# Kernel optimization log

Hardware: AMD Instinct MI355X
Metric: run time of the kernel (lower is better)

Reference implementation:

```python
import jax, jax.numpy as jnp
import numpy as np

BN_EPS = 1e-5

def setup_inputs() -> dict:
    key = jax.random.key(0)
    ks = jax.random.split(key, 6)
    N, D, H = 1024, 256, 128
    scale = 0.05
    return {
        "graph_embeddings": jax.random.normal(ks[0], (N, D), jnp.float32),
        "W1": jax.random.normal(ks[1], (2 * D, H), jnp.float32) * scale,
        "b1": jnp.zeros((H,), jnp.float32),
        "W2": jax.random.normal(ks[2], (H, 1), jnp.float32) * scale,
        "b2": jnp.zeros((1,), jnp.float32),
        "Wg": jax.random.normal(ks[3], (D, H), jnp.float32) * scale,
        "bg": jnp.zeros((H,), jnp.float32),
        "gamma": jnp.ones((H,), jnp.float32),
        "beta": jnp.zeros((H,), jnp.float32),
    }

def reference(graph_embeddings, W1, b1, W2, b2, Wg, bg, gamma, beta):
    N, D = graph_embeddings.shape
    # Pairwise similarity MLP: sim(i,j) = sigmoid(W2 @ relu(W1 @ [x_i; x_j] + b1) + b2)
    # Split W1 over the concat dim so we never materialize [N,N,2D].
    a = graph_embeddings @ W1[:D]          # [N, H] contribution of x_i
    c = graph_embeddings @ W1[D:]          # [N, H] contribution of x_j
    h = jax.nn.relu(a[:, None, :] + c[None, :, :] + b1)   # [N, N, H]
    sim = jax.nn.sigmoid(jnp.einsum('ijh,h->ij', h, W2[:, 0]) + b2[0])  # [N, N]
    # Torch loop uses sim(i,j) with i<j for both directions; keep edge iff sim > 0.5.
    U = jnp.triu(sim, k=1)
    A = jnp.where(U > 0.5, U, 0.0)
    A = A + A.T + jnp.eye(N, dtype=sim.dtype)  # symmetric + GCN self-loops (weight 1)
    # GCN symmetric normalization: D^{-1/2} A D^{-1/2}
    deg = A.sum(axis=1)
    dis = jax.lax.rsqrt(deg)
    A_hat = A * dis[:, None] * dis[None, :]
    out = A_hat @ (graph_embeddings @ Wg) + bg  # [N, H]
    # BatchNorm1d (training mode: batch stats, biased variance)
    mean = out.mean(axis=0)
    var = out.var(axis=0)
    out = gamma * (out - mean) * jax.lax.rsqrt(var + BN_EPS) + beta
    return jax.nn.relu(out)
```

## Files before the change

kernel.cpp:

```cpp
#include <hip/hip_runtime.h>
#include <math.h>

constexpr int NN = 1024;
constexpr int DD = 256;
constexpr int HH = 128;
constexpr float BN_EPS = 1e-5f;

constexpr int OFF_A      = 0;
constexpr int OFF_AP     = OFF_A + NN * NN;
constexpr int OFF_CP     = OFF_AP + NN * HH;
constexpr int OFF_Y      = OFF_CP + NN * HH;
constexpr int OFF_DEG    = OFF_Y + NN * HH;
constexpr int OFF_P0     = OFF_DEG + NN;
constexpr int OFF_P1     = OFF_P0 + NN * HH;

__global__ __launch_bounds__(256) void k1_gemm(
    const float* __restrict__ X, const float* __restrict__ W1,
    const float* __restrict__ Wg, const float* __restrict__ b1,
    float* __restrict__ aP, float* __restrict__ cP, float* __restrict__ Y,
    float* __restrict__ deg) {
  const int tid = threadIdx.x;
  const int blk = blockIdx.x;
  if (blk >= 192) {
    for (int i = tid; i < NN; i += 256) deg[i] = 0.f;
    return;
  }
  __shared__ float xs[16 * 256];
  __shared__ float ws[64 * 128];
  const int i0 = (blk & 63) * 16;
  const int m = blk >> 6;
  const float* W = (m == 0) ? W1 : (m == 1 ? W1 + DD * HH : Wg);
  const float* Xbase = X + i0 * DD;
#pragma unroll
  for (int v = 0; v < 4; ++v) {
    const int fi = (v * 256 + tid) * 4;
    *(float4*)(xs + fi) = *(const float4*)(Xbase + fi);
  }
  const int tx = tid & 31, ty = tid >> 5;
  float4 acc0 = make_float4(0.f, 0.f, 0.f, 0.f);
  float4 acc1 = make_float4(0.f, 0.f, 0.f, 0.f);
  for (int c = 0; c < 4; ++c) {
    __syncthreads();
    const float* Wbase = W + c * 64 * HH;
#pragma unroll
    for (int v = 0; v < 8; ++v) {
      const int fi = (v * 256 + tid) * 4;
      *(float4*)(ws + fi) = *(const float4*)(Wbase + fi);
    }
    __syncthreads();
    const float* xr0 = xs + (ty * 2) * 256 + c * 64;
    const float* xr1 = xs + (ty * 2 + 1) * 256 + c * 64;
#pragma unroll 4
    for (int d = 0; d < 64; d += 4) {
      const float4 x0 = *(const float4*)(xr0 + d);
      const float4 x1 = *(const float4*)(xr1 + d);
      const float4 w0 = *(const float4*)(ws + (d + 0) * 128 + tx * 4);
      const float4 w1 = *(const float4*)(ws + (d + 1) * 128 + tx * 4);
      const float4 w2 = *(const float4*)(ws + (d + 2) * 128 + tx * 4);
      const float4 w3 = *(const float4*)(ws + (d + 3) * 128 + tx * 4);
      acc0.x = fmaf(x0.x, w0.x, acc0.x); acc0.y = fmaf(x0.x, w0.y, acc0.y);
      acc0.z = fmaf(x0.x, w0.z, acc0.z); acc0.w = fmaf(x0.x, w0.w, acc0.w);
      acc1.x = fmaf(x1.x, w0.x, acc1.x); acc1.y = fmaf(x1.x, w0.y, acc1.y);
      acc1.z = fmaf(x1.x, w0.z, acc1.z); acc1.w = fmaf(x1.x, w0.w, acc1.w);
      acc0.x = fmaf(x0.y, w1.x, acc0.x); acc0.y = fmaf(x0.y, w1.y, acc0.y);
      acc0.z = fmaf(x0.y, w1.z, acc0.z); acc0.w = fmaf(x0.y, w1.w, acc0.w);
      acc1.x = fmaf(x1.y, w1.x, acc1.x); acc1.y = fmaf(x1.y, w1.y, acc1.y);
      acc1.z = fmaf(x1.y, w1.z, acc1.z); acc1.w = fmaf(x1.y, w1.w, acc1.w);
      acc0.x = fmaf(x0.z, w2.x, acc0.x); acc0.y = fmaf(x0.z, w2.y, acc0.y);
      acc0.z = fmaf(x0.z, w2.z, acc0.z); acc0.w = fmaf(x0.z, w2.w, acc0.w);
      acc1.x = fmaf(x1.z, w2.x, acc1.x); acc1.y = fmaf(x1.z, w2.y, acc1.y);
      acc1.z = fmaf(x1.z, w2.z, acc1.z); acc1.w = fmaf(x1.z, w2.w, acc1.w);
      acc0.x = fmaf(x0.w, w3.x, acc0.x); acc0.y = fmaf(x0.w, w3.y, acc0.y);
      acc0.z = fmaf(x0.w, w3.z, acc0.z); acc0.w = fmaf(x0.w, w3.w, acc0.w);
      acc1.x = fmaf(x1.w, w3.x, acc1.x); acc1.y = fmaf(x1.w, w3.y, acc1.y);
      acc1.z = fmaf(x1.w, w3.z, acc1.z); acc1.w = fmaf(x1.w, w3.w, acc1.w);
    }
  }
  float* dst = (m == 0) ? aP : (m == 1 ? cP : Y);
  if (m == 0) {
    const float4 bv = *(const float4*)(b1 + tx * 4);
    acc0.x += bv.x; acc0.y += bv.y; acc0.z += bv.z; acc0.w += bv.w;
    acc1.x += bv.x; acc1.y += bv.y; acc1.z += bv.z; acc1.w += bv.w;
  }
  const int r0 = i0 + ty * 2;
  *(float4*)(dst + r0 * HH + tx * 4) = acc0;
  *(float4*)(dst + (r0 + 1) * HH + tx * 4) = acc1;
}

__global__ __launch_bounds__(256) void k2_pairwise(
    const float* __restrict__ aP, const float* __restrict__ cP,
    const float* __restrict__ W2, const float* __restrict__ b2,
    float* __restrict__ A, float* __restrict__ deg) {
  __shared__ float as[32 * 132];
  __shared__ float cs[32 * 132];
  __shared__ float es[32 * 33];
  __shared__ float ws2[128];
  const int tid = threadIdx.x;
  int tt = blockIdx.x, ti = 0;
  while (tt >= 32 - ti) { tt -= 32 - ti; ++ti; }
  const int tj = ti + tt;
  const int i0 = ti * 32, j0 = tj * 32;
  if (tid < 32) *(float4*)(ws2 + tid * 4) = *(const float4*)(W2 + tid * 4);
  for (int idx = tid; idx < 32 * HH; idx += 256) {
    const int row = idx >> 7, col = idx & 127;
    as[row * 132 + col] = aP[(i0 + row) * HH + col];
    cs[row * 132 + col] = cP[(j0 + row) * HH + col];
  }
  __syncthreads();
  const int li0 = (tid >> 4) * 2, lj0 = (tid & 15) * 2;
  float s00 = 0.f, s01 = 0.f, s10 = 0.f, s11 = 0.f;
#pragma unroll 8
  for (int h = 0; h < HH; h += 4) {
    const float4 a0 = *(const float4*)(as + li0 * 132 + h);
    const float4 a1 = *(const float4*)(as + (li0 + 1) * 132 + h);
    const float4 c0 = *(const float4*)(cs + lj0 * 132 + h);
    const float4 c1 = *(const float4*)(cs + (lj0 + 1) * 132 + h);
    const float4 w = *(const float4*)(ws2 + h);
    s00 += fmaxf(a0.x + c0.x, 0.f) * w.x + fmaxf(a0.y + c0.y, 0.f) * w.y +
           fmaxf(a0.z + c0.z, 0.f) * w.z + fmaxf(a0.w + c0.w, 0.f) * w.w;
    s01 += fmaxf(a0.x + c1.x, 0.f) * w.x + fmaxf(a0.y + c1.y, 0.f) * w.y +
           fmaxf(a0.z + c1.z, 0.f) * w.z + fmaxf(a0.w + c1.w, 0.f) * w.w;
    s10 += fmaxf(a1.x + c0.x, 0.f) * w.x + fmaxf(a1.y + c0.y, 0.f) * w.y +
           fmaxf(a1.z + c0.z, 0.f) * w.z + fmaxf(a1.w + c0.w, 0.f) * w.w;
    s11 += fmaxf(a1.x + c1.x, 0.f) * w.x + fmaxf(a1.y + c1.y, 0.f) * w.y +
           fmaxf(a1.z + c1.z, 0.f) * w.z + fmaxf(a1.w + c1.w, 0.f) * w.w;
  }
  const float b2v = b2[0];
  auto edge = [b2v](float s) {
    s += b2v;
    return s > 0.f ? 1.f / (1.f + __expf(-s)) : 0.f;
  };
  es[(li0 + 0) * 33 + lj0 + 0] = edge(s00);
  es[(li0 + 0) * 33 + lj0 + 1] = edge(s01);
  es[(li0 + 1) * 33 + lj0 + 0] = edge(s10);
  es[(li0 + 1) * 33 + lj0 + 1] = edge(s11);
  __syncthreads();
  if (ti == tj) {
    float f[2][2];
#pragma unroll
    for (int r = 0; r < 2; ++r)
#pragma unroll
      for (int c = 0; c < 2; ++c) {
        const int li = li0 + r, lj = lj0 + c;
        f[r][c] =
            (li == lj) ? 1.f : (li < lj ? es[li * 33 + lj] : es[lj * 33 + li]);
      }
    __syncthreads();
    es[(li0 + 0) * 33 + lj0 + 0] = f[0][0];
    es[(li0 + 0) * 33 + lj0 + 1] = f[0][1];
    es[(li0 + 1) * 33 + lj0 + 0] = f[1][0];
    es[(li0 + 1) * 33 + lj0 + 1] = f[1][1];
    __syncthreads();
  }
  if (tid < 32) {
    float s = 0.f;
#pragma unroll
    for (int c = 0; c < 32; ++c) s += es[tid * 33 + c];
    atomicAdd(deg + i0 + tid, s);
  } else if (tid < 64 && ti != tj) {
    const int c = tid - 32;
    float s = 0.f;
#pragma unroll
    for (int r = 0; r < 32; ++r) s += es[r * 33 + c];
    atomicAdd(deg + j0 + c, s);
  }
#pragma unroll
  for (int r = 0; r < 2; ++r)
#pragma unroll
    for (int c = 0; c < 2; ++c) {
      const int li = li0 + r, lj = lj0 + c;
      A[(i0 + li) * NN + j0 + lj] = es[li * 33 + lj];
      if (ti != tj) A[(j0 + li) * NN + i0 + lj] = es[lj * 33 + li];
    }
}

__global__ __launch_bounds__(256) void k3_spmm(
    const float* __restrict__ A, const float* __restrict__ Y,
    const float* __restrict__ deg, float* __restrict__ P0,
    float* __restrict__ P1) {
  __shared__ float Ast[512 * 12];
  __shared__ float disl[NN];
  __shared__ float red[8 * 1032];
  const int tid = threadIdx.x;
  const int rb = blockIdx.x >> 1, half = blockIdx.x & 1;
  const int i0 = rb * 8, jh0 = half * 512;
  float* __restrict__ P = half ? P1 : P0;
  {
    const float4 dv = *(const float4*)(deg + tid * 4);
    float4 r;
    r.x = rsqrtf(dv.x); r.y = rsqrtf(dv.y);
    r.z = rsqrtf(dv.z); r.w = rsqrtf(dv.w);
    *(float4*)(disl + tid * 4) = r;
  }
  __syncthreads();
#pragma unroll
  for (int v = 0; v < 2; ++v) {
    const int jj = v * 256 + tid;
    const int jg = jh0 + jj;
    const float d = disl[jg];
    float a[8];
#pragma unroll
    for (int r = 0; r < 8; ++r) a[r] = A[(i0 + r) * NN + jg] * d;
    *(float4*)(Ast + jj * 12)     = make_float4(a[0], a[1], a[2], a[3]);
    *(float4*)(Ast + jj * 12 + 4) = make_float4(a[4], a[5], a[6], a[7]);
  }
  __syncthreads();
  const int tx = tid & 31, ty = tid >> 5;
  const int jj0 = ty * 64;
  float4 acc[8];
#pragma unroll
  for (int r = 0; r < 8; ++r) acc[r] = make_float4(0.f, 0.f, 0.f, 0.f);
  const float* Yb = Y + (jh0 + jj0) * HH + tx * 4;
#define FMA4(AC, S) \
  AC.x = fmaf(S, yv.x, AC.x); AC.y = fmaf(S, yv.y, AC.y); \
  AC.z = fmaf(S, yv.z, AC.z); AC.w = fmaf(S, yv.w, AC.w);
#pragma unroll 4
  for (int jj = 0; jj < 64; ++jj) {
    const float4 yv = *(const float4*)(Yb + jj * HH);
    const float4 lo = *(const float4*)(Ast + (jj0 + jj) * 12);
    const float4 hi = *(const float4*)(Ast + (jj0 + jj) * 12 + 4);
    FMA4(acc[0], lo.x) FMA4(acc[1], lo.y) FMA4(acc[2], lo.z) FMA4(acc[3], lo.w)
    FMA4(acc[4], hi.x) FMA4(acc[5], hi.y) FMA4(acc[6], hi.z) FMA4(acc[7], hi.w)
  }
#undef FMA4
#pragma unroll
  for (int r = 0; r < 8; ++r)
    *(float4*)(red + ty * 1032 + r * 128 + tx * 4) = acc[r];
  __syncthreads();
  const int h = tid & 127, rg = tid >> 7;
  float* Pcol = P + h * NN + i0;
#pragma unroll
  for (int k = 0; k < 4; ++k) {
    const int row = rg + 2 * k;
    float v = 0.f;
#pragma unroll
    for (int t = 0; t < 8; ++t) v += red[t * 1032 + row * 128 + h];
    Pcol[row] = v * disl[i0 + row];
  }
}

__global__ __launch_bounds__(256) void k4_bn(
    const float* __restrict__ P0, const float* __restrict__ P1,
    const float* __restrict__ bg, const float* __restrict__ gamma,
    const float* __restrict__ beta, float* __restrict__ out) {
  const int tid = threadIdx.x, h = blockIdx.x;
  const float bgv = bg[h];
  const float4 p0 = *(const float4*)(P0 + h * NN + tid * 4);
  const float4 p1 = *(const float4*)(P1 + h * NN + tid * 4);
  float v[4] = {p0.x + p1.x + bgv, p0.y + p1.y + bgv,
                p0.z + p1.z + bgv, p0.w + p1.w + bgv};
  float s1 = v[0] + v[1] + v[2] + v[3];
  float s2 = v[0] * v[0] + v[1] * v[1] + v[2] * v[2] + v[3] * v[3];
  __shared__ float rs1[4], rs2[4], msh[2];
#pragma unroll
  for (int off = 32; off; off >>= 1) {
    s1 += __shfl_down(s1, off);
    s2 += __shfl_down(s2, off);
  }
  if ((tid & 63) == 0) { rs1[tid >> 6] = s1; rs2[tid >> 6] = s2; }
  __syncthreads();
  if (tid == 0) {
    const float t1 = rs1[0] + rs1[1] + rs1[2] + rs1[3];
    const float t2 = rs2[0] + rs2[1] + rs2[2] + rs2[3];
    const float mean = t1 * (1.f / NN);
    const float var = t2 * (1.f / NN) - mean * mean;
    msh[0] = mean;
    msh[1] = rsqrtf(var + BN_EPS);
  }
  __syncthreads();
  const float mean = msh[0], rinv = msh[1];
  const float g = gamma[h], be = beta[h];
#pragma unroll
  for (int k = 0; k < 4; ++k) {
    const float val = g * (v[k] - mean) * rinv + be;
    out[(tid * 4 + k) * HH + h] = fmaxf(val, 0.f);
  }
}

extern "C" void kernel_launch(void* const* d_in, const int* in_sizes, int n_in,
                              void* d_out, int out_size, void* d_ws,
                              size_t ws_size, hipStream_t stream) {
  const float* X = (const float*)d_in[0];
  const float* W1 = (const float*)d_in[1];
  const float* b1 = (const float*)d_in[2];
  const float* W2 = (const float*)d_in[3];
  const float* b2 = (const float*)d_in[4];
  const float* Wg = (const float*)d_in[5];
  const float* bg = (const float*)d_in[6];
  const float* gamma = (const float*)d_in[7];
  const float* beta = (const float*)d_in[8];
  float* out = (float*)d_out;

  float* w = (float*)d_ws;
  float* A = w + OFF_A;
  float* aP = w + OFF_AP;
  float* cP = w + OFF_CP;
  float* Y = w + OFF_Y;
  float* deg = w + OFF_DEG;
  float* P0 = w + OFF_P0;
  float* P1 = w + OFF_P1;

  k1_gemm<<<dim3(193), 256, 0, stream>>>(X, W1, Wg, b1, aP, cP, Y, deg);
  k2_pairwise<<<dim3(528), 256, 0, stream>>>(aP, cP, W2, b2, A, deg);
  k3_spmm<<<dim3(256), 256, 0, stream>>>(A, Y, deg, P0, P1);
  k4_bn<<<dim3(128), 256, 0, stream>>>(P0, P1, bg, gamma, beta, out);
}
```

Measured before the change: 110.9 us.

## Fuse four kernels into one persistent kernel with grid-wide atomic barriers

Merges the GEMM, pairwise-similarity, aggregation and batch-norm kernels into one 256-block kernel whose stages are separated by software grid barriers built from atomic counters. A memset clears the barrier counters before each launch. The pairwise stage now loops over its 528 tiles with a stride of 256 blocks and loads tiles with float4 copies. This removes three kernel launch gaps, but it relies on all 256 blocks being resident at once and adds the cost of the barrier spins plus an extra memset operation.

Measured after the change: 192.6 us. +73.6%, slower.

```diff
diff --git a/kernel.cpp b/kernel.cpp
--- a/kernel.cpp
+++ b/kernel.cpp
@@ -13,267 +13,291 @@
 constexpr int OFF_DEG    = OFF_Y + NN * HH;
 constexpr int OFF_P0     = OFF_DEG + NN;
 constexpr int OFF_P1     = OFF_P0 + NN * HH;
-
-__global__ __launch_bounds__(256) void k1_gemm(
+constexpr int OFF_BAR    = OFF_P1 + NN * HH;
+
+constexpr int GRID = 256;
+
+__device__ __forceinline__ void grid_barrier(int* bar) {
+  __syncthreads();
+  if (threadIdx.x == 0) {
+    __threadfence();
+    __hip_atomic_fetch_add(bar, 1, __ATOMIC_RELEASE, __HIP_MEMORY_SCOPE_AGENT);
+    while (__hip_atomic_load(bar, __ATOMIC_ACQUIRE,
+                             __HIP_MEMORY_SCOPE_AGENT) < GRID) {
+      __builtin_amdgcn_s_sleep(8);
+    }
+  }
+  __syncthreads();
+}
+
+__global__ __launch_bounds__(256) void fused_all(
     const float* __restrict__ X, const float* __restrict__ W1,
-    const float* __restrict__ Wg, const float* __restrict__ b1,
-    float* __restrict__ aP, float* __restrict__ cP, float* __restrict__ Y,
-    float* __restrict__ deg) {
+    const float* __restrict__ b1, const float* __restrict__ W2,
+    const float* __restrict__ b2, const float* __restrict__ Wg,
+    const float* __restrict__ bg, const float* __restrict__ gamma,
+    const float* __restrict__ beta, float* __restrict__ out,
+    float* __restrict__ A, float* __restrict__ aP, float* __restrict__ cP,
+    float* __restrict__ Y, float* __restrict__ deg, float* __restrict__ P0,
+    float* __restrict__ P1, int* __restrict__ bar) {
+  __shared__ float smem[15424];
   const int tid = threadIdx.x;
-  const int blk = blockIdx.x;
-  if (blk >= 192) {
+  const int bid = blockIdx.x;
+
+  if (bid < 192) {
+    float* xs = smem;
+    float* ws = smem + 4096;
+    const int i0 = (bid & 63) * 16;
+    const int m = bid >> 6;
+    const float* W = (m == 0) ? W1 : (m == 1 ? W1 + DD * HH : Wg);
+    const float* Xbase = X + i0 * DD;
+#pragma unroll
+    for (int v = 0; v < 4; ++v) {
+      const int fi = (v * 256 + tid) * 4;
+      *(float4*)(xs + fi) = *(const float4*)(Xbase + fi);
+    }
+    const int tx = tid & 31, ty = tid >> 5;
+    float4 acc0 = make_float4(0.f, 0.f, 0.f, 0.f);
+    float4 acc1 = make_float4(0.f, 0.f, 0.f, 0.f);
+    for (int c = 0; c < 4; ++c) {
+      __syncthreads();
+      const float* Wbase = W + c * 64 * HH;
+#pragma unroll
+      for (int v = 0; v < 8; ++v) {
+        const int fi = (v * 256 + tid) * 4;
+        *(float4*)(ws + fi) = *(const float4*)(Wbase + fi);
+      }
+      __syncthreads();
+      const float* xr0 = xs + (ty * 2) * 256 + c * 64;
+      const float* xr1 = xs + (ty * 2 + 1) * 256 + c * 64;
+#pragma unroll 4
+      for (int d = 0; d < 64; d += 4) {
+        const float4 x0 = *(const float4*)(xr0 + d);
+        const float4 x1 = *(const float4*)(xr1 + d);
+        const float4 w0 = *(const float4*)(ws + (d + 0) * 128 + tx * 4);
+        const float4 w1 = *(const float4*)(ws + (d + 1) * 128 + tx * 4);
+        const float4 w2 = *(const float4*)(ws + (d + 2) * 128 + tx * 4);
+        const float4 w3 = *(const float4*)(ws + (d + 3) * 128 + tx * 4);
+        acc0.x = fmaf(x0.x, w0.x, acc0.x); acc0.y = fmaf(x0.x, w0.y, acc0.y);
+        acc0.z = fmaf(x0.x, w0.z, acc0.z); acc0.w = fmaf(x0.x, w0.w, acc0.w);
+        acc1.x = fmaf(x1.x, w0.x, acc1.x); acc1.y = fmaf(x1.x, w0.y, acc1.y);
+        acc1.z = fmaf(x1.x, w0.z, acc1.z); acc1.w = fmaf(x1.x, w0.w, acc1.w);
+        acc0.x = fmaf(x0.y, w1.x, acc0.x); acc0.y = fmaf(x0.y, w1.y, acc0.y);
+        acc0.z = fmaf(x0.y, w1.z, acc0.z); acc0.w = fmaf(x0.y, w1.w, acc0.w);
+        acc1.x = fmaf(x1.y, w1.x, acc1.x); acc1.y = fmaf(x1.y, w1.y, acc1.y);
+        acc1.z = fmaf(x1.y, w1.z, acc1.z); acc1.w = fmaf(x1.y, w1.w, acc1.w);
+        acc0.x = fmaf(x0.z, w2.x, acc0.x); acc0.y = fmaf(x0.z, w2.y, acc0.y);
+        acc0.z = fmaf(x0.z, w2.z, acc0.z); acc0.w = fmaf(x0.z, w2.w, acc0.w);
+        acc1.x = fmaf(x1.z, w2.x, acc1.x); acc1.y = fmaf(x1.z, w2.y, acc1.y);
+        acc1.z = fmaf(x1.z, w2.z, acc1.z); acc1.w = fmaf(x1.z, w2.w, acc1.w);
+        acc0.x = fmaf(x0.w, w3.x, acc0.x); acc0.y = fmaf(x0.w, w3.y, acc0.y);
+        acc0.z = fmaf(x0.w, w3.z, acc0.z); acc0.w = fmaf(x0.w, w3.w, acc0.w);
+        acc1.x = fmaf(x1.w, w3.x, acc1.x); acc1.y = fmaf(x1.w, w3.y, acc1.y);
+        acc1.z = fmaf(x1.w, w3.z, acc1.z); acc1.w = fmaf(x1.w, w3.w, acc1.w);
+      }
+    }
+    float* dst = (m == 0) ? aP : (m == 1 ? cP : Y);
+    if (m == 0) {
+      const float4 bv = *(const float4*)(b1 + tx * 4);
+      acc0.x += bv.x; acc0.y += bv.y; acc0.z += bv.z; acc0.w += bv.w;
+      acc1.x += bv.x; acc1.y += bv.y; acc1.z += bv.z; acc1.w += bv.w;
+    }
+    const int r0 = i0 + ty * 2;
+    *(float4*)(dst + r0 * HH + tx * 4) = acc0;
+    *(float4*)(dst + (r0 + 1) * HH + tx * 4) = acc1;
+  } else if (bid == 192) {
     for (int i = tid; i < NN; i += 256) deg[i] = 0.f;
-    return;
-  }
-  __shared__ float xs[16 * 256];
-  __shared__ float ws[64 * 128];
-  const int i0 = (blk & 63) * 16;
-  const int m = blk >> 6;
-  const float* W = (m == 0) ? W1 : (m == 1 ? W1 + DD * HH : Wg);
-  const float* Xbase = X + i0 * DD;
-#pragma unroll
-  for (int v = 0; v < 4; ++v) {
-    const int fi = (v * 256 + tid) * 4;
-    *(float4*)(xs + fi) = *(const float4*)(Xbase + fi);
-  }
-  const int tx = tid & 31, ty = tid >> 5;
-  float4 acc0 = make_float4(0.f, 0.f, 0.f, 0.f);
-  float4 acc1 = make_float4(0.f, 0.f, 0.f, 0.f);
-  for (int c = 0; c < 4; ++c) {
-    __syncthreads();
-    const float* Wbase = W + c * 64 * HH;
-#pragma unroll
-    for (int v = 0; v < 8; ++v) {
-      const int fi = (v * 256 + tid) * 4;
-      *(float4*)(ws + fi) = *(const float4*)(Wbase + fi);
-    }
-    __syncthreads();
-    const float* xr0 = xs + (ty * 2) * 256 + c * 64;
-    const float* xr1 = xs + (ty * 2 + 1) * 256 + c * 64;
-#pragma unroll 4
-    for (int d = 0; d < 64; d += 4) {
-      const float4 x0 = *(const float4*)(xr0 + d);
-      const float4 x1 = *(const float4*)(xr1 + d);
-      const float4 w0 = *(const float4*)(ws + (d + 0) * 128 + tx * 4);
-      const float4 w1 = *(const float4*)(ws + (d + 1) * 128 + tx * 4);
-      const float4 w2 = *(const float4*)(ws + (d + 2) * 128 + tx * 4);
-      const float4 w3 = *(const float4*)(ws + (d + 3) * 128 + tx * 4);
-      acc0.x = fmaf(x0.x, w0.x, acc0.x); acc0.y = fmaf(x0.x, w0.y, acc0.y);
-      acc0.z = fmaf(x0.x, w0.z, acc0.z); acc0.w = fmaf(x0.x, w0.w, acc0.w);
-      acc1.x = fmaf(x1.x, w0.x, acc1.x); acc1.y = fmaf(x1.x, w0.y, acc1.y);
-      acc1.z = fmaf(x1.x, w0.z, acc1.z); acc1.w = fmaf(x1.x, w0.w, acc1.w);
-      acc0.x = fmaf(x0.y, w1.x, acc0.x); acc0.y = fmaf(x0.y, w1.y, acc0.y);
-      acc0.z = fmaf(x0.y, w1.z, acc0.z); acc0.w = fmaf(x0.y, w1.w, acc0.w);
-      acc1.x = fmaf(x1.y, w1.x, acc1.x); acc1.y = fmaf(x1.y, w1.y, acc1.y);
-      acc1.z = fmaf(x1.y, w1.z, acc1.z); acc1.w = fmaf(x1.y, w1.w, acc1.w);
-      acc0.x = fmaf(x0.z, w2.x, acc0.x); acc0.y = fmaf(x0.z, w2.y, acc0.y);
-      acc0.z = fmaf(x0.z, w2.z, acc0.z); acc0.w = fmaf(x0.z, w2.w, acc0.w);
-      acc1.x = fmaf(x1.z, w2.x, acc1.x); acc1.y = fmaf(x1.z, w2.y, acc1.y);
-      acc1.z = fmaf(x1.z, w2.z, acc1.z); acc1.w = fmaf(x1.z, w2.w, acc1.w);
-      acc0.x = fmaf(x0.w, w3.x, acc0.x); acc0.y = fmaf(x0.w, w3.y, acc0.y);
-      acc0.z = fmaf(x0.w, w3.z, acc0.z); acc0.w = fmaf(x0.w, w3.w, acc0.w);
-      acc1.x = fmaf(x1.w, w3.x, acc1.x); acc1.y = fmaf(x1.w, w3.y, acc1.y);
-      acc1.z = fmaf(x1.w, w3.z, acc1.z); acc1.w = fmaf(x1.w, w3.w, acc1.w);
-    }
-  }
-  float* dst = (m == 0) ? aP : (m == 1 ? cP : Y);
-  if (m == 0) {
-    const float4 bv = *(const float4*)(b1 + tx * 4);
-    acc0.x += bv.x; acc0.y += bv.y; acc0.z += bv.z; acc0.w += bv.w;
-    acc1.x += bv.x; acc1.y += bv.y; acc1.z += bv.z; acc1.w += bv.w;
-  }
-  const int r0 = i0 + ty * 2;
-  *(float4*)(dst + r0 * HH + tx * 4) = acc0;
-  *(float4*)(dst + (r0 + 1) * HH + tx * 4) = acc1;
-}
-
-__global__ __launch_bounds__(256) void k2_pairwise(
-    const float* __restrict__ aP, const float* __restrict__ cP,
-    const float* __restrict__ W2, const float* __restrict__ b2,
-    float* __restrict__ A, float* __restrict__ deg) {
-  __shared__ float as[32 * 132];
-  __shared__ float cs[32 * 132];
-  __shared__ float es[32 * 33];
-  __shared__ float ws2[128];
-  const int tid = threadIdx.x;
-  int tt = blockIdx.x, ti = 0;
-  while (tt >= 32 - ti) { tt -= 32 - ti; ++ti; }
-  const int tj = ti + tt;
-  const int i0 = ti * 32, j0 = tj * 32;
-  if (tid < 32) *(float4*)(ws2 + tid * 4) = *(const float4*)(W2 + tid * 4);
-  for (int idx = tid; idx < 32 * HH; idx += 256) {
-    const int row = idx >> 7, col = idx & 127;
-    as[row * 132 + col] = aP[(i0 + row) * HH + col];
-    cs[row * 132 + col] = cP[(j0 + row) * HH + col];
-  }
-  __syncthreads();
-  const int li0 = (tid >> 4) * 2, lj0 = (tid & 15) * 2;
-  float s00 = 0.f, s01 = 0.f, s10 = 0.f, s11 = 0.f;
+  }
+  grid_barrier(bar + 0);
+
+  {
+    float* as  = smem;
+    float* cs  = smem + 4224;
+    float* es  = smem + 8448;
+    float* ws2 = smem + 9504;
+    if (tid < 32) *(float4*)(ws2 + tid * 4) = *(const float4*)(W2 + tid * 4);
+    const int li0 = (tid >> 4) * 2, lj0 = (tid & 15) * 2;
+    for (int t = bid; t < 528; t += 256) {
+      int tt = t, ti = 0;
+      while (tt >= 32 - ti) { tt -= 32 - ti; ++ti; }
+      const int tj = ti + tt;
+      const int i0 = ti * 32, j0 = tj * 32;
+      __syncthreads();
+#pragma unroll
+      for (int v = 0; v < 4; ++v) {
+        const int f = v * 256 + tid;
+        const int row = f >> 5, c4 = (f & 31) * 4;
+        *(float4*)(as + row * 132 + c4) =
+            *(const float4*)(aP + (i0 + row) * HH + c4);
+        *(float4*)(cs + row * 132 + c4) =
+            *(const float4*)(cP + (j0 + row) * HH + c4);
+      }
+      __syncthreads();
+      float s00 = 0.f, s01 = 0.f, s10 = 0.f, s11 = 0.f;
 #pragma unroll 8
-  for (int h = 0; h < HH; h += 4) {
-    const float4 a0 = *(const float4*)(as + li0 * 132 + h);
-    const float4 a1 = *(const float4*)(as + (li0 + 1) * 132 + h);
-    const float4 c0 = *(const float4*)(cs + lj0 * 132 + h);
-    const float4 c1 = *(const float4*)(cs + (lj0 + 1) * 132 + h);
-    const float4 w = *(const float4*)(ws2 + h);
-    s00 += fmaxf(a0.x + c0.x, 0.f) * w.x + fmaxf(a0.y + c0.y, 0.f) * w.y +
-           fmaxf(a0.z + c0.z, 0.f) * w.z + fmaxf(a0.w + c0.w, 0.f) * w.w;
-    s01 += fmaxf(a0.x + c1.x, 0.f) * w.x + fmaxf(a0.y + c1.y, 0.f) * w.y +
-           fmaxf(a0.z + c1.z, 0.f) * w.z + fmaxf(a0.w + c1.w, 0.f) * w.w;
-    s10 += fmaxf(a1.x + c0.x, 0.f) * w.x + fmaxf(a1.y + c0.y, 0.f) * w.y +
-           fmaxf(a1.z + c0.z, 0.f) * w.z + fmaxf(a1.w + c0.w, 0.f) * w.w;
-    s11 += fmaxf(a1.x + c1.x, 0.f) * w.x + fmaxf(a1.y + c1.y, 0.f) * w.y +
-           fmaxf(a1.z + c1.z, 0.f) * w.z + fmaxf(a1.w + c1.w, 0.f) * w.w;
-  }
-  const float b2v = b2[0];
-  auto edge = [b2v](float s) {
-    s += b2v;
-    return s > 0.f ? 1.f / (1.f + __expf(-s)) : 0.f;
-  };
-  es[(li0 + 0) * 33 + lj0 + 0] = edge(s00);
-  es[(li0 + 0) * 33 + lj0 + 1] = edge(s01);
-  es[(li0 + 1) * 33 + lj0 + 0] = edge(s10);
-  es[(li0 + 1) * 33 + lj0 + 1] = edge(s11);
-  __syncthreads();
-  if (ti == tj) {
-    float f[2][2];
-#pragma unroll
-    for (int r = 0; r < 2; ++r)
-#pragma unroll
-      for (int c = 0; c < 2; ++c) {
-        const int li = li0 + r, lj = lj0 + c;
-        f[r][c] =
-            (li == lj) ? 1.f : (li < lj ? es[li * 33 + lj] : es[lj * 33 + li]);
-      }
-    __syncthreads();
-    es[(li0 + 0) * 33 + lj0 + 0] = f[0][0];
-    es[(li0 + 0) * 33 + lj0 + 1] = f[0][1];
-    es[(li0 + 1) * 33 + lj0 + 0] = f[1][0];
-    es[(li0 + 1) * 33 + lj0 + 1] = f[1][1];
-    __syncthreads();
-  }
-  if (tid < 32) {
-    float s = 0.f;
-#pragma unroll
-    for (int c = 0; c < 32; ++c) s += es[tid * 33 + c];
-    atomicAdd(deg + i0 + tid, s);
-  } else if (tid < 64 && ti != tj) {
-    const int c = tid - 32;
-    float s = 0.f;
-#pragma unroll
-    for (int r = 0; r < 32; ++r) s += es[r * 33 + c];
-    atomicAdd(deg + j0 + c, s);
-  }
-#pragma unroll
-  for (int r = 0; r < 2; ++r)
-#pragma unroll
-    for (int c = 0; c < 2; ++c) {
-      const int li = li0 + r, lj = lj0 + c;
-      A[(i0 + li) * NN + j0 + lj] = es[li * 33 + lj];
-      if (ti != tj) A[(j0 + li) * NN + i0 + lj] = es[lj * 33 + li];
-    }
-}
-
-__global__ __launch_bounds__(256) void k3_spmm(
-    const float* __restrict__ A, const float* __restrict__ Y,
-    const float* __restrict__ deg, float* __restrict__ P0,
-    float* __restrict__ P1) {
-  __shared__ float Ast[512 * 12];
-  __shared__ float disl[NN];
-  __shared__ float red[8 * 1032];
-  const int tid = threadIdx.x;
-  const int rb = blockIdx.x >> 1, half = blockIdx.x & 1;
-  const int i0 = rb * 8, jh0 = half * 512;
-  float* __restrict__ P = half ? P1 : P0;
+      for (int h = 0; h < HH; h += 4) {
+        const float4 a0 = *(const float4*)(as + li0 * 132 + h);
+        const float4 a1 = *(const float4*)(as + (li0 + 1) * 132 + h);
+        const float4 c0 = *(const float4*)(cs + lj0 * 132 + h);
+        const float4 c1 = *(const float4*)(cs + (lj0 + 1) * 132 + h);
+        const float4 w = *(const float4*)(ws2 + h);
+        s00 += fmaxf(a0.x + c0.x, 0.f) * w.x + fmaxf(a0.y + c0.y, 0.f) * w.y +
+               fmaxf(a0.z + c0.z, 0.f) * w.z + fmaxf(a0.w + c0.w, 0.f) * w.w;
+        s01 += fmaxf(a0.x + c1.x, 0.f) * w.x + fmaxf(a0.y + c1.y, 0.f) * w.y +
+               fmaxf(a0.z + c1.z, 0.f) * w.z + fmaxf(a0.w + c1.w, 0.f) * w.w;
+        s10 += fmaxf(a1.x + c0.x, 0.f) * w.x + fmaxf(a1.y + c0.y, 0.f) * w.y +
+               fmaxf(a1.z + c0.z, 0.f) * w.z + fmaxf(a1.w + c0.w, 0.f) * w.w;
+        s11 += fmaxf(a1.x + c1.x, 0.f) * w.x + fmaxf(a1.y + c1.y, 0.f) * w.y +
+               fmaxf(a1.z + c1.z, 0.f) * w.z + fmaxf(a1.w + c1.w, 0.f) * w.w;
+      }
+      const float b2v = b2[0];
+      auto edge = [b2v](float s) {
+        s += b2v;
+        return s > 0.f ? 1.f / (1.f + __expf(-s)) : 0.f;
+      };
+      es[(li0 + 0) * 33 + lj0 + 0] = edge(s00);
+      es[(li0 + 0) * 33 + lj0 + 1] = edge(s01);
+      es[(li0 + 1) * 33 + lj0 + 0] = edge(s10);
+      es[(li0 + 1) * 33 + lj0 + 1] = edge(s11);
+      __syncthreads();
+      if (ti == tj) {
+        float f[2][2];
+#pragma unroll
+        for (int r = 0; r < 2; ++r)
+#pragma unroll
+          for (int c = 0; c < 2; ++c) {
+            const int li = li0 + r, lj = lj0 + c;
+            f[r][c] = (li == lj)
+                          ? 1.f
+                          : (li < lj ? es[li * 33 + lj] : es[lj * 33 + li]);
+          }
+        __syncthreads();
+        es[(li0 + 0) * 33 + lj0 + 0] = f[0][0];
+        es[(li0 + 0) * 33 + lj0 + 1] = f[0][1];
+        es[(li0 + 1) * 33 + lj0 + 0] = f[1][0];
+        es[(li0 + 1) * 33 + lj0 + 1] = f[1][1];
+        __syncthreads();
+      }
+      if (tid < 32) {
+        float s = 0.f;
+#pragma unroll
+        for (int c = 0; c < 32; ++c) s += es[tid * 33 + c];
+        atomicAdd(deg + i0 + tid, s);
+      } else if (tid < 64 && ti != tj) {
+        const int c = tid - 32;
+        float s = 0.f;
+#pragma unroll
+        for (int r = 0; r < 32; ++r) s += es[r * 33 + c];
+        atomicAdd(deg + j0 + c, s);
+      }
+#pragma unroll
+      for (int r = 0; r < 2; ++r)
+#pragma unroll
+        for (int c = 0; c < 2; ++c) {
+          const int li = li0 + r, lj = lj0 + c;
+          A[(i0 + li) * NN + j0 + lj] = es[li * 33 + lj];
+          if (ti != tj) A[(j0 + li) * NN + i0 + lj] = es[lj * 33 + li];
+        }
+    }
+  }
+  grid_barrier(bar + 1);
+
   {
-    const float4 dv = *(const float4*)(deg + tid * 4);
-    float4 r;
-    r.x = rsqrtf(dv.x); r.y = rsqrtf(dv.y);
-    r.z = rsqrtf(dv.z); r.w = rsqrtf(dv.w);
-    *(float4*)(disl + tid * 4) = r;
-  }
-  __syncthreads();
-#pragma unroll
-  for (int v = 0; v < 2; ++v) {
-    const int jj = v * 256 + tid;
-    const int jg = jh0 + jj;
-    const float d = disl[jg];
-    float a[8];
-#pragma unroll
-    for (int r = 0; r < 8; ++r) a[r] = A[(i0 + r) * NN + jg] * d;
-    *(float4*)(Ast + jj * 12)     = make_float4(a[0], a[1], a[2], a[3]);
-    *(float4*)(Ast + jj * 12 + 4) = make_float4(a[4], a[5], a[6], a[7]);
-  }
-  __syncthreads();
-  const int tx = tid & 31, ty = tid >> 5;
-  const int jj0 = ty * 64;
-  float4 acc[8];
-#pragma unroll
-  for (int r = 0; r < 8; ++r) acc[r] = make_float4(0.f, 0.f, 0.f, 0.f);
-  const float* Yb = Y + (jh0 + jj0) * HH + tx * 4;
+    float* Ast  = smem;
+    float* disl = smem + 6144;
+    float* red  = smem + 7168;
+    const int rb = bid >> 1, half = bid & 1;
+    const int i0 = rb * 8, jh0 = half * 512;
+    float* __restrict__ P = half ? P1 : P0;
+    {
+      const float4 dv = *(const float4*)(deg + tid * 4);
+      float4 r;
+      r.x = rsqrtf(dv.x); r.y = rsqrtf(dv.y);
+      r.z = rsqrtf(dv.z); r.w = rsqrtf(dv.w);
+      *(float4*)(disl + tid * 4) = r;
+    }
+    __syncthreads();
+#pragma unroll
+    for (int v = 0; v < 2; ++v) {
+      const int jj = v * 256 + tid;
+      const int jg = jh0 + jj;
+      const float d = disl[jg];
+      float a[8];
+#pragma unroll
+      for (int r = 0; r < 8; ++r) a[r] = A[(i0 + r) * NN + jg] * d;
+      *(float4*)(Ast + jj * 12)     = make_float4(a[0], a[1], a[2], a[3]);
+      *(float4*)(Ast + jj * 12 + 4) = make_float4(a[4], a[5], a[6], a[7]);
+    }
+    __syncthreads();
+    const int tx = tid & 31, ty = tid >> 5;
+    const int jj0 = ty * 64;
+    float4 acc[8];
+#pragma unroll
+    for (int r = 0; r < 8; ++r) acc[r] = make_float4(0.f, 0.f, 0.f, 0.f);
+    const float* Yb = Y + (jh0 + jj0) * HH + tx * 4;
 #define FMA4(AC, S) \
   AC.x = fmaf(S, yv.x, AC.x); AC.y = fmaf(S, yv.y, AC.y); \
   AC.z = fmaf(S, yv.z, AC.z); AC.w = fmaf(S, yv.w, AC.w);
 #pragma unroll 4
-  for (int jj = 0; jj < 64; ++jj) {
-    const float4 yv = *(const float4*)(Yb + jj * HH);
-    const float4 lo = *(const float4*)(Ast + (jj0 + jj) * 12);
-    const float4 hi = *(const float4*)(Ast + (jj0 + jj) * 12 + 4);
-    FMA4(acc[0], lo.x) FMA4(acc[1], lo.y) FMA4(acc[2], lo.z) FMA4(acc[3], lo.w)
-    FMA4(acc[4], hi.x) FMA4(acc[5], hi.y) FMA4(acc[6], hi.z) FMA4(acc[7], hi.w)
-  }
+    for (int jj = 0; jj < 64; ++jj) {
+      const float4 yv = *(const float4*)(Yb + jj * HH);
+      const float4 lo = *(const float4*)(Ast + (jj0 + jj) * 12);
+      const float4 hi = *(const float4*)(Ast + (jj0 + jj) * 12 + 4);
+      FMA4(acc[0], lo.x) FMA4(acc[1], lo.y) FMA4(acc[2], lo.z) FMA4(acc[3], lo.w)
+      FMA4(acc[4], hi.x) FMA4(acc[5], hi.y) FMA4(acc[6], hi.z) FMA4(acc[7], hi.w)
+    }
 #undef FMA4
 #pragma unroll
-  for (int r = 0; r < 8; ++r)
-    *(float4*)(red + ty * 1032 + r * 128 + tx * 4) = acc[r];
-  __syncthreads();
-  const int h = tid & 127, rg = tid >> 7;
-  float* Pcol = P + h * NN + i0;
-#pragma unroll
-  for (int k = 0; k < 4; ++k) {
-    const int row = rg + 2 * k;
-    float v = 0.f;
-#pragma unroll
-    for (int t = 0; t < 8; ++t) v += red[t * 1032 + row * 128 + h];
-    Pcol[row] = v * disl[i0 + row];
-  }
-}
-
-__global__ __launch_bounds__(256) void k4_bn(
-    const float* __restrict__ P0, const float* __restrict__ P1,
-    const float* __restrict__ bg, const float* __restrict__ gamma,
-    const float* __restrict__ beta, float* __restrict__ out) {
-  const int tid = threadIdx.x, h = blockIdx.x;
-  const float bgv = bg[h];
-  const float4 p0 = *(const float4*)(P0 + h * NN + tid * 4);
-  const float4 p1 = *(const float4*)(P1 + h * NN + tid * 4);
-  float v[4] = {p0.x + p1.x + bgv, p0.y + p1.y + bgv,
-                p0.z + p1.z + bgv, p0.w + p1.w + bgv};
-  float s1 = v[0] + v[1] + v[2] + v[3];
-  float s2 = v[0] * v[0] + v[1] * v[1] + v[2] * v[2] + v[3] * v[3];
-  __shared__ float rs1[4], rs2[4], msh[2];
-#pragma unroll
-  for (int off = 32; off; off >>= 1) {
-    s1 += __shfl_down(s1, off);
-    s2 += __shfl_down(s2, off);
-  }
-  if ((tid & 63) == 0) { rs1[tid >> 6] = s1; rs2[tid >> 6] = s2; }
-  __syncthreads();
-  if (tid == 0) {
-    const float t1 = rs1[0] + rs1[1] + rs1[2] + rs1[3];
-    const float t2 = rs2[0] + rs2[1] + rs2[2] + rs2[3];
-    const float mean = t1 * (1.f / NN);
-    const float var = t2 * (1.f / NN) - mean * mean;
-    msh[0] = mean;
-    msh[1] = rsqrtf(var + BN_EPS);
-  }
-  __syncthreads();
-  const float mean = msh[0], rinv = msh[1];
-  const float g = gamma[h], be = beta[h];
-#pragma unroll
-  for (int k = 0; k < 4; ++k) {
-    const float val = g * (v[k] - mean) * rinv + be;
-    out[(tid * 4 + k) * HH + h] = fmaxf(val, 0.f);
+    for (int r = 0; r < 8; ++r)
+      *(float4*)(red + ty * 1032 + r * 128 + tx * 4) = acc[r];
+    __syncthreads();
+    const int h = tid & 127, rg = tid >> 7;
+    float* Pcol = P + h * NN + i0;
+#pragma unroll
+    for (int k = 0; k < 4; ++k) {
+      const int row = rg + 2 * k;
+      float v = 0.f;
+#pragma unroll
+      for (int t = 0; t < 8; ++t) v += red[t * 1032 + row * 128 + h];
+      Pcol[row] = v * disl[i0 + row];
+    }
+  }
+  grid_barrier(bar + 2);
+
+  if (bid < 128) {
+    float* rs1 = smem;
+    float* rs2 = smem + 4;
+    float* msh = smem + 8;
+    const int h = bid;
+    const float bgv = bg[h];
+    const float4 p0 = *(const float4*)(P0 + h * NN + tid * 4);
+    const float4 p1 = *(const float4*)(P1 + h * NN + tid * 4);
+    float v[4] = {p0.x + p1.x + bgv, p0.y + p1.y + bgv,
+                  p0.z + p1.z + bgv, p0.w + p1.w + bgv};
+    float s1 = v[0] + v[1] + v[2] + v[3];
+    float s2 = v[0] * v[0] + v[1] * v[1] + v[2] * v[2] + v[3] * v[3];
+#pragma unroll
+    for (int off = 32; off; off >>= 1) {
+      s1 += __shfl_down(s1, off);
+      s2 += __shfl_down(s2, off);
+    }
+    if ((tid & 63) == 0) { rs1[tid >> 6] = s1; rs2[tid >> 6] = s2; }
+    __syncthreads();
+    if (tid == 0) {
+      const float t1 = rs1[0] + rs1[1] + rs1[2] + rs1[3];
+      const float t2 = rs2[0] + rs2[1] + rs2[2] + rs2[3];
+      const float mean = t1 * (1.f / NN);
+      const float var = t2 * (1.f / NN) - mean * mean;
+      msh[0] = mean;
+      msh[1] = rsqrtf(var + BN_EPS);
+    }
+    __syncthreads();
+    const float mean = msh[0], rinv = msh[1];
+    const float g = gamma[h], be = beta[h];
+#pragma unroll
+    for (int k = 0; k < 4; ++k) {
+      const float val = g * (v[k] - mean) * rinv + be;
+      out[(tid * 4 + k) * HH + h] = fmaxf(val, 0.f);
+    }
   }
 }
 
@@ -299,9 +323,10 @@
   float* deg = w + OFF_DEG;
   float* P0 = w + OFF_P0;
   float* P1 = w + OFF_P1;
-
-  k1_gemm<<<dim3(193), 256, 0, stream>>>(X, W1, Wg, b1, aP, cP, Y, deg);
-  k2_pairwise<<<dim3(528), 256, 0, stream>>>(aP, cP, W2, b2, A, deg);
-  k3_spmm<<<dim3(256), 256, 0, stream>>>(A, Y, deg, P0, P1);
-  k4_bn<<<dim3(128), 256, 0, stream>>>(P0, P1, bg, gamma, beta, out);
+  int* bar = (int*)(w + OFF_BAR);
+
+  hipMemsetAsync(bar, 0, 3 * sizeof(int), stream);
+  fused_all<<<dim3(GRID), dim3(256), 0, stream>>>(
+      X, W1, b1, W2, b2, Wg, bg, gamma, beta, out, A, aP, cP, Y, deg, P0, P1,
+      bar);
 }
```
